# Performance work log

Hardware: AMD Instinct MI355X
Metric: run time of the kernel (lower is better)

The kernel has to match this reference:

```python
import jax, jax.numpy as jnp
import numpy as np

TAU = 1.0          # temperature
PAD = -1.0         # padded_value_indicator
MAX_ITER = 50      # sinkhorn iterations
NEG_BIG = -100000000.0


def setup_inputs() -> dict:
    key = jax.random.key(0)
    k1, k2 = jax.random.split(key)
    B, N = 128, 256
    y_pred = jax.random.normal(k1, (B, N), dtype=jnp.float32)
    y_true = jax.random.randint(k2, (B, N), 0, 5, dtype=jnp.int32)
    return {"y_pred": y_pred, "y_true": y_true}


def deterministic_neural_sort(s, tau, mask):
    # s: [B, n, 1], mask: [B, n] bool
    B, n = s.shape[0], s.shape[1]
    mor = mask[:, :, None] | mask[:, None, :]
    mand = mask[:, :, None] & mask[:, None, :]
    s = jnp.where(mask[:, :, None], NEG_BIG, s)
    A_s = jnp.abs(s - jnp.swapaxes(s, 1, 2))            # [B, n, n]
    A_s = jnp.where(mor, 0.0, A_s)
    # B_mat[b,i,j] = sum_k A_s[b,i,k] (matmul with ones outer product)
    B_mat = A_s.sum(axis=2, keepdims=True)              # [B, n, 1], broadcasts over j
    m = mask.sum(axis=1)                                # [B] number of padded items
    j = jnp.arange(n)
    valid = j[None, :] < (n - m)[:, None]
    scaling = jnp.where(
        valid,
        (n - m)[:, None].astype(jnp.float32) + 1.0 - 2.0 * (j[None, :] + 1).astype(jnp.float32),
        0.0,
    )                                                   # [B, n]
    s0 = jnp.where(mask[:, :, None], 0.0, s)
    C = s0 * scaling[:, None, :]                        # [B,n,1]*[B,1,n] outer product
    P_max = jnp.swapaxes(C - B_mat, 1, 2)
    P_max = jnp.where(mor, -jnp.inf, P_max)
    P_max = jnp.where(mand, 1.0, P_max)
    return jax.nn.softmax(P_max / tau, axis=-1)         # [B, n, n]


def sinkhorn_scaling(mat, mask):
    # mat: [B, n, n], mask: [B, n]
    mor = mask[:, None, :] | mask[:, :, None]
    mand = mask[:, None, :] & mask[:, :, None]
    mat = jnp.where(mor, 0.0, mat)
    mat = jnp.where(mand, 1.0, mat)

    def step(m, _):
        m = m / jnp.clip(m.sum(axis=1, keepdims=True), 1e-10, None)
        m = m / jnp.clip(m.sum(axis=2, keepdims=True), 1e-10, None)
        return m, None

    mat, _ = jax.lax.scan(step, mat, None, length=MAX_ITER)
    return jnp.where(mor, 0.0, mat)


def dcg_at_k(y_pred, y_true, k, gain_fn):
    # returns [B, 1]
    mask = y_true == PAD
    yp = jnp.where(mask, -jnp.inf, y_pred)
    yt = jnp.where(mask, 0.0, y_true)
    order = jnp.argsort(-yp, axis=-1)
    sorted_true = jnp.take_along_axis(yt, order, axis=-1)
    n = y_true.shape[1]
    disc = 1.0 / jnp.log2(jnp.arange(n, dtype=jnp.float32) + 2.0)
    cum = jnp.cumsum(gain_fn(sorted_true) * disc, axis=1)[:, :k]
    return cum[:, k - 1 : k]


def reference(y_pred, y_true):
    B, n = y_pred.shape
    yt = y_true.astype(jnp.float32)
    yt = yt.max() - yt + yt.min()            # relevancy flip as in source
    k = n                                    # self.k is None
    mask = yt == PAD

    P_hat = deterministic_neural_sort(y_pred[:, :, None], TAU, mask)  # [B,n,n]
    P_hat = sinkhorn_scaling(P_hat, mask)[None]                        # [1,B,n,n]
    mor = mask[None, :, :, None] | mask[None, :, None, :]
    P_hat = jnp.where(mor, 0.0, P_hat)

    yt_masked = jnp.where(mask, 0.0, yt)
    gains = jnp.power(2.0, yt_masked) - 1.0                            # powered_relevancies
    ground_truth = jnp.einsum('sbij,bj->sbi', P_hat, gains)            # [1,B,n]
    disc = 1.0 / jnp.log2(jnp.arange(n, dtype=jnp.float32) + 2.0)
    discounted_gains = ground_truth * disc

    idcg = dcg_at_k(yt, yt, k, lambda x: jnp.power(2.0, x) - 1.0).T    # [1,B]
    ndcg = discounted_gains[:, :, :k].sum(axis=-1) / (idcg + 1e-10)    # [1,B]
    idcg_mask = idcg == 0.0
    ndcg = jnp.where(idcg_mask, 0.0, ndcg)
    cnt = (~idcg_mask).sum()
    mean_ndcg = ndcg.sum() / jnp.maximum(cnt.astype(jnp.float32) * ndcg.shape[0], 1.0)
    return jnp.where(cnt > 0, -mean_ndcg, 0.0)
```

## Files before the change

kernel.cpp:

```cpp
#include <hip/hip_runtime.h>


#define NN 256
#define ITERS 50

typedef float v2f __attribute__((ext_vector_type(2)));

__device__ __forceinline__ v2f pkfma(v2f a, v2f b, v2f c) {
    return __builtin_elementwise_fma(a, b, c);
}

template<int C>
__device__ __forceinline__ float dppadd(float v) {
    return v + __int_as_float(__builtin_amdgcn_update_dpp(0, __float_as_int(v), C, 0xF, 0xF, true));
}
template<int C>
__device__ __forceinline__ float dppmax(float v) {
    return fmaxf(v, __int_as_float(__builtin_amdgcn_update_dpp(0, __float_as_int(v), C, 0xF, 0xF, true)));
}
__device__ __forceinline__ float swz16(float v) {
    return __int_as_float(__builtin_amdgcn_ds_swizzle(__float_as_int(v), 0x401F));
}
__device__ __forceinline__ float sum16(float v) {
    v = dppadd<0xB1>(v);
    v = dppadd<0x4E>(v);
    v = dppadd<0x141>(v);
    v = dppadd<0x140>(v);
    return v;
}
__device__ __forceinline__ float sum32f(float v) {
    v = sum16(v);
    v += swz16(v);
    return v;
}
__device__ __forceinline__ float max32f(float v) {
    v = dppmax<0xB1>(v);
    v = dppmax<0x4E>(v);
    v = dppmax<0x141>(v);
    v = dppmax<0x140>(v);
    v = fmaxf(v, swz16(v));
    return v;
}

#if __has_builtin(__builtin_amdgcn_permlane16_swap)
#define HAVE_PLS 1
#endif

__device__ __forceinline__ void sum32_pair(float& A, float& B) {
    A = sum16(A);
    B = sum16(B);
#ifdef HAVE_PLS
    auto r1 = __builtin_amdgcn_permlane16_swap(__float_as_uint(A), __float_as_uint(B), false, false);
    float z = __uint_as_float(r1[0]) + __uint_as_float(r1[1]);
    auto r2 = __builtin_amdgcn_permlane16_swap(__float_as_uint(z), __float_as_uint(z), false, false);
    A = __uint_as_float(r2[0]);
    B = __uint_as_float(r2[1]);
#else
    A += swz16(A);
    B += swz16(B);
#endif
}

__global__ __launch_bounds__(1024, 4) void ndcg_main(const float* __restrict__ yp,
                                                     const int* __restrict__ ytr,
                                                     int nbatch,
                                                     float* __restrict__ ndArr,
                                                     float* __restrict__ cntArr,
                                                     int* __restrict__ doneCnt,
                                                     float* __restrict__ out) {
    const int b = blockIdx.x;
    const int t = threadIdx.x;
    const int l = t & 63;
    const int ti = t >> 5;
    const int tj = t & 31;
    const int cq = t >> 4;
    const int sl = t & 15;

    __shared__ float4 part4[32 * 64];
    __shared__ float4 cvec4[72];
    __shared__ __align__(16) float sarr[NN], bmarr[NN], garr[NN], darr[NN];
    __shared__ float numAcc, idcgAcc;
    __shared__ int hist[64], wmn[16], wmx[16], gmn, gmx;
    __shared__ float redS[16], redC[16];
    __shared__ int lastFlag;

    float* partf = (float*)part4;

    {
        int mn = 0x7fffffff, mx = (int)0x80000000;
        const int4* y4 = (const int4*)ytr;
        const int n4 = nbatch * (NN / 4);
        for (int i = t; i < n4; i += 1024) {
            int4 v = y4[i];
            mn = min(mn, min(min(v.x, v.y), min(v.z, v.w)));
            mx = max(mx, max(max(v.x, v.y), max(v.z, v.w)));
        }
        for (int mo = 1; mo < 64; mo <<= 1) {
            mn = min(mn, __shfl_xor(mn, mo));
            mx = max(mx, __shfl_xor(mx, mo));
        }
        if (l == 0) { wmn[t >> 6] = mn; wmx[t >> 6] = mx; }
    }
    if (t < 64) hist[t] = 0;
    if (t < 72) cvec4[t] = make_float4(1.0f, 1.0f, 1.0f, 1.0f);
    if (t == 0) { numAcc = 0.0f; idcgAcc = 0.0f; }
    __syncthreads();
    if (t == 0) {
        int a = wmn[0], c = wmx[0];
        for (int i = 1; i < 16; ++i) { a = min(a, wmn[i]); c = max(c, wmx[i]); }
        gmn = a; gmx = c;
    }
    __syncthreads();
    const int ymin = gmn, ymax = gmx;

    if (t < NN) {
        sarr[t] = yp[b * NN + t];
        int ytv = ymax - ytr[b * NN + t] + ymin;
        garr[t] = exp2f((float)ytv) - 1.0f;
        darr[t] = 1.0f / log2f((float)t + 2.0f);
        atomicAdd(&hist[min(max(ytv - ymin, 0), 63)], 1);
    }
    __syncthreads();

    {
        int j = t & 255, q = t >> 8;
        float sv = sarr[j];
        float acc = 0.0f;
        int k0 = q * 64;
#pragma unroll 8
        for (int k = 0; k < 64; ++k) acc += fabsf(sv - sarr[k0 + k]);
        partf[q * 256 + j] = acc;
    }
    __syncthreads();
    if (t < NN)
        bmarr[t] = partf[t] + partf[256 + t] + partf[512 + t] + partf[768 + t];
    __syncthreads();

    v2f m2[8][4];
    {
        float sj[8], bm8[8];
        *(float4*)&sj[0]  = ((const float4*)sarr)[tj * 2];
        *(float4*)&sj[4]  = ((const float4*)sarr)[tj * 2 + 1];
        *(float4*)&bm8[0] = ((const float4*)bmarr)[tj * 2];
        *(float4*)&bm8[4] = ((const float4*)bmarr)[tj * 2 + 1];
#pragma unroll
        for (int a = 0; a < 8; ++a) {
            float sc = (float)(255 - 2 * (ti * 8 + a));
            float mv[8];
            float mx = -3.0e38f;
#pragma unroll
            for (int bb = 0; bb < 8; ++bb) {
                mv[bb] = sj[bb] * sc - bm8[bb];
                mx = fmaxf(mx, mv[bb]);
            }
            mx = max32f(mx);
            float z = 0.0f;
#pragma unroll
            for (int bb = 0; bb < 8; ++bb) { mv[bb] = expf(mv[bb] - mx); z += mv[bb]; }
            z = sum32f(z);
            float rz = __builtin_amdgcn_rcpf(z);
#pragma unroll
            for (int bb = 0; bb < 8; ++bb) m2[a][bb >> 1][bb & 1] = mv[bb] * rz;
        }
    }

    if (t < NN) {
        float gain_p = 0.0f;
        int off = 0;
        for (int vb = 63; vb >= 0; --vb) {
            int c = hist[vb];
            if (t >= off && t < off + c) gain_p = exp2f((float)(vb + ymin)) - 1.0f;
            off += c;
        }
        float contrib = sum32f(darr[t] * gain_p);
        contrib += __shfl_xor(contrib, 32);
        if (l == 0) atomicAdd(&idcgAcc, contrib);
    }

    float r[8];
#pragma unroll
    for (int a = 0; a < 8; ++a) r[a] = 1.0f;

    const int wslot = ti * 64 + ((tj + ti) & 31);
    const int csc = t >> 5;
    const int hh = cq & 1;
    const int rslot1 = sl * 64 + ((csc + sl) & 31) + 32 * hh;
    const int rslot2 = (sl + 16) * 64 + ((csc + sl + 16) & 31) + 32 * hh;
    const int cwslot = cq + (cq >> 3);
    const int crslot = tj * 2 + (tj >> 2);

    {
        v2f p2[4];
#pragma unroll
        for (int bp = 0; bp < 4; ++bp)
            p2[bp] = ((m2[0][bp] + m2[1][bp]) + (m2[2][bp] + m2[3][bp])) +
                     ((m2[4][bp] + m2[5][bp]) + (m2[6][bp] + m2[7][bp]));
        part4[wslot]      = make_float4(p2[0].x, p2[0].y, p2[1].x, p2[1].y);
        part4[wslot + 32] = make_float4(p2[2].x, p2[2].y, p2[3].x, p2[3].y);
    }

    for (int it = 0; it < ITERS; ++it) {
        __syncthreads();
        {
            float4 A0 = part4[rslot1];
            float4 A1 = part4[rslot2];
            v2f s01 = (v2f){A0.x, A0.y} + (v2f){A1.x, A1.y};
            v2f s23 = (v2f){A0.z, A0.w} + (v2f){A1.z, A1.w};
            float Sx = sum16(s01.x);
            float Sy = sum16(s01.y);
            float Sz = sum16(s23.x);
            float Sw = sum16(s23.y);
            if (sl == 0) {
                float4 C = cvec4[cwslot];
                float4 F;
                F.x = C.x * __builtin_amdgcn_rcpf(fmaxf(C.x * Sx, 1e-10f));
                F.y = C.y * __builtin_amdgcn_rcpf(fmaxf(C.y * Sy, 1e-10f));
                F.z = C.z * __builtin_amdgcn_rcpf(fmaxf(C.z * Sz, 1e-10f));
                F.w = C.w * __builtin_amdgcn_rcpf(fmaxf(C.w * Sw, 1e-10f));
                cvec4[cwslot] = F;
            }
        }
        __syncthreads();

        {
            float4 ca = cvec4[crslot];
            float4 cb = cvec4[crslot + 1];
            v2f cv2[4] = { {ca.x, ca.y}, {ca.z, ca.w}, {cb.x, cb.y}, {cb.z, cb.w} };
            float rs[8];
#pragma unroll
            for (int a = 0; a < 8; ++a) {
                v2f acc = m2[a][0] * cv2[0];
                acc = pkfma(m2[a][1], cv2[1], acc);
                acc = pkfma(m2[a][2], cv2[2], acc);
                acc = pkfma(m2[a][3], cv2[3], acc);
                rs[a] = acc.x + acc.y;
            }
            sum32_pair(rs[0], rs[1]);
            sum32_pair(rs[2], rs[3]);
            sum32_pair(rs[4], rs[5]);
            sum32_pair(rs[6], rs[7]);
#pragma unroll
            for (int a = 0; a < 8; ++a) {
                float T = fmaxf(r[a] * rs[a], 1e-10f);
                r[a] *= __builtin_amdgcn_rcpf(T);
            }
            v2f p2[4];
#pragma unroll
            for (int bp = 0; bp < 4; ++bp) {
                v2f rr = r[0];
                v2f acc = m2[0][bp] * rr;
#pragma unroll
                for (int a = 1; a < 8; ++a) {
                    v2f ra = r[a];
                    acc = pkfma(m2[a][bp], ra, acc);
                }
                p2[bp] = acc;
            }
            part4[wslot]      = make_float4(p2[0].x, p2[0].y, p2[1].x, p2[1].y);
            part4[wslot + 32] = make_float4(p2[2].x, p2[2].y, p2[3].x, p2[3].y);
        }
    }

    {
        float4 fa = cvec4[crslot];
        float4 fb = cvec4[crslot + 1];
        float4 ga = ((const float4*)garr)[tj * 2];
        float4 gb = ((const float4*)garr)[tj * 2 + 1];
        v2f gv2[4] = { (v2f){fa.x, fa.y} * (v2f){ga.x, ga.y},
                       (v2f){fa.z, fa.w} * (v2f){ga.z, ga.w},
                       (v2f){fb.x, fb.y} * (v2f){gb.x, gb.y},
                       (v2f){fb.z, fb.w} * (v2f){gb.z, gb.w} };
        float q[8];
#pragma unroll
        for (int a = 0; a < 8; ++a) {
            v2f acc = m2[a][0] * gv2[0];
            acc = pkfma(m2[a][1], gv2[1], acc);
            acc = pkfma(m2[a][2], gv2[2], acc);
            acc = pkfma(m2[a][3], gv2[3], acc);
            q[a] = acc.x + acc.y;
        }
        sum32_pair(q[0], q[1]);
        sum32_pair(q[2], q[3]);
        sum32_pair(q[4], q[5]);
        sum32_pair(q[6], q[7]);
        float partial = 0.0f;
#pragma unroll
        for (int a = 0; a < 8; ++a)
            partial = fmaf(darr[ti * 8 + a] * r[a], q[a], partial);
        if (tj == 0) atomicAdd(&numAcc, partial);
    }
    __syncthreads();

    if (t == 0) {
        float idcg = idcgAcc;
        bool ok = (idcg != 0.0f);
        float nd = ok ? numAcc / (idcg + 1e-10f) : 0.0f;
        __hip_atomic_store(&ndArr[b], nd, __ATOMIC_RELAXED, __HIP_MEMORY_SCOPE_AGENT);
        __hip_atomic_store(&cntArr[b], ok ? 1.0f : 0.0f, __ATOMIC_RELAXED, __HIP_MEMORY_SCOPE_AGENT);
        __threadfence();
        int prev = atomicAdd(doneCnt, 1);
        lastFlag = (prev == nbatch - 1) ? 1 : 0;
    }
    __syncthreads();
    if (lastFlag != 0) {
        __threadfence();
        float s = 0.0f, c = 0.0f;
        for (int i = t; i < nbatch; i += 1024) {
            s += __hip_atomic_load(&ndArr[i], __ATOMIC_RELAXED, __HIP_MEMORY_SCOPE_AGENT);
            c += __hip_atomic_load(&cntArr[i], __ATOMIC_RELAXED, __HIP_MEMORY_SCOPE_AGENT);
        }
        for (int mo = 1; mo < 64; mo <<= 1) { s += __shfl_xor(s, mo); c += __shfl_xor(c, mo); }
        if (l == 0) { redS[t >> 6] = s; redC[t >> 6] = c; }
        __syncthreads();
        if (t == 0) {
            float S = 0.0f, C = 0.0f;
            for (int i = 0; i < 16; ++i) { S += redS[i]; C += redC[i]; }
            out[0] = (C > 0.0f) ? -(S / fmaxf(C, 1.0f)) : 0.0f;
        }
    }
}

extern "C" void kernel_launch(void* const* d_in, const int* in_sizes, int n_in,
                              void* d_out, int out_size, void* d_ws, size_t ws_size,
                              hipStream_t stream) {
    const float* y_pred = (const float*)d_in[0];
    const int* y_true = (const int*)d_in[1];
    const int total = in_sizes[0];
    const int B = total / NN;

    int* doneCnt = (int*)d_ws;
    float* ndArr = (float*)d_ws + 64;
    float* cntArr = ndArr + B;

    hipMemsetAsync(doneCnt, 0, sizeof(int), stream);
    ndcg_main<<<B, 1024, 0, stream>>>(y_pred, y_true, B, ndArr, cntArr, doneCnt,
                                      (float*)d_out);
}
```

Measured before the change: 161.7 us.

## Exit Sinkhorn iterations early once scaling vectors reach a bitwise fixed point

The 50 Sinkhorn iterations are split into 12 unconditional iterations, then chunks of four. Each chunk snapshots the row and column scaling vectors after its second iteration and compares them bitwise after its fourth. If every thread sees identical values, the block leaves the loop, because any further iterations would only reproduce the same state. Otherwise it finishes the remaining two iterations, for 50 in total. This is meant to cut the per-iteration barrier and reduction cost when the scalings settle early. It adds snapshot storage in registers and shared memory, plus an extra barrier and wave vote per chunk.

```diff
diff --git a/kernel.cpp b/kernel.cpp
--- a/kernel.cpp
+++ b/kernel.cpp
@@ -60,6 +60,96 @@
     B += swz16(B);
 #endif
 }
+
+#define SINK_B_PHASE                                                         \
+    {                                                                        \
+        float4 A0 = part4[rslot1];                                           \
+        float4 A1 = part4[rslot2];                                           \
+        v2f s01 = (v2f){A0.x, A0.y} + (v2f){A1.x, A1.y};                     \
+        v2f s23 = (v2f){A0.z, A0.w} + (v2f){A1.z, A1.w};                     \
+        float Sx = sum16(s01.x);                                             \
+        float Sy = sum16(s01.y);                                             \
+        float Sz = sum16(s23.x);                                             \
+        float Sw = sum16(s23.y);                                             \
+        if (sl == 0) {                                                       \
+            float4 C = cvec4[cwslot];                                        \
+            float4 F;                                                        \
+            F.x = C.x * __builtin_amdgcn_rcpf(fmaxf(C.x * Sx, 1e-10f));      \
+            F.y = C.y * __builtin_amdgcn_rcpf(fmaxf(C.y * Sy, 1e-10f));      \
+            F.z = C.z * __builtin_amdgcn_rcpf(fmaxf(C.z * Sz, 1e-10f));      \
+            F.w = C.w * __builtin_amdgcn_rcpf(fmaxf(C.w * Sw, 1e-10f));      \
+            cvec4[cwslot] = F;                                               \
+        }                                                                    \
+    }
+
+#define SINK_CA_PHASE(EXTRA)                                                 \
+    {                                                                        \
+        float4 ca = cvec4[crslot];                                           \
+        float4 cb = cvec4[crslot + 1];                                       \
+        v2f cv2[4] = { {ca.x, ca.y}, {ca.z, ca.w}, {cb.x, cb.y}, {cb.z, cb.w} }; \
+        float rs[8];                                                         \
+        _Pragma("unroll")                                                    \
+        for (int a = 0; a < 8; ++a) {                                        \
+            v2f acc = m2[a][0] * cv2[0];                                     \
+            acc = pkfma(m2[a][1], cv2[1], acc);                              \
+            acc = pkfma(m2[a][2], cv2[2], acc);                              \
+            acc = pkfma(m2[a][3], cv2[3], acc);                              \
+            rs[a] = acc.x + acc.y;                                           \
+        }                                                                    \
+        sum32_pair(rs[0], rs[1]);                                            \
+        sum32_pair(rs[2], rs[3]);                                            \
+        sum32_pair(rs[4], rs[5]);                                            \
+        sum32_pair(rs[6], rs[7]);                                            \
+        _Pragma("unroll")                                                    \
+        for (int a = 0; a < 8; ++a) {                                        \
+            float T = fmaxf(r[a] * rs[a], 1e-10f);                           \
+            r[a] *= __builtin_amdgcn_rcpf(T);                                \
+        }                                                                    \
+        EXTRA                                                                \
+        {                                                                    \
+            v2f p2[4];                                                       \
+            _Pragma("unroll")                                                \
+            for (int bp = 0; bp < 4; ++bp) {                                 \
+                v2f rr = r[0];                                               \
+                v2f acc = m2[0][bp] * rr;                                    \
+                _Pragma("unroll")                                            \
+                for (int a = 1; a < 8; ++a) {                                \
+                    v2f ra = r[a];                                           \
+                    acc = pkfma(m2[a][bp], ra, acc);                         \
+                }                                                            \
+                p2[bp] = acc;                                                \
+            }                                                                \
+            part4[wslot]      = make_float4(p2[0].x, p2[0].y, p2[1].x, p2[1].y); \
+            part4[wslot + 32] = make_float4(p2[2].x, p2[2].y, p2[3].x, p2[3].y); \
+        }                                                                    \
+    }
+
+#define SINK_ITER(EXTRA) { __syncthreads(); SINK_B_PHASE; __syncthreads(); SINK_CA_PHASE(EXTRA) }
+
+#define SNAP_EXTRA                                                           \
+    {                                                                        \
+        _Pragma("unroll")                                                    \
+        for (int a = 0; a < 8; ++a) rsnap[a] = r[a];                         \
+        if (t < 72) csnap[t] = cvec4[t];                                     \
+    }
+
+#define CHECK_EXTRA                                                          \
+    {                                                                        \
+        bool okc = true;                                                     \
+        _Pragma("unroll")                                                    \
+        for (int a = 0; a < 8; ++a)                                          \
+            okc &= (__float_as_uint(r[a]) == __float_as_uint(rsnap[a]));     \
+        if (t < 72) {                                                        \
+            float4 Aq = cvec4[t];                                            \
+            float4 Bq = csnap[t];                                            \
+            okc &= (__float_as_uint(Aq.x) == __float_as_uint(Bq.x));         \
+            okc &= (__float_as_uint(Aq.y) == __float_as_uint(Bq.y));         \
+            okc &= (__float_as_uint(Aq.z) == __float_as_uint(Bq.z));         \
+            okc &= (__float_as_uint(Aq.w) == __float_as_uint(Bq.w));         \
+        }                                                                    \
+        if (!__all(okc) && l == 0) convFlag[ci & 1] = 0;                     \
+        if (t == 0) convFlag[(ci + 1) & 1] = 1;                              \
+    }
 
 __global__ __launch_bounds__(1024, 4) void ndcg_main(const float* __restrict__ yp,
                                                      const int* __restrict__ ytr,
@@ -78,11 +168,13 @@
 
     __shared__ float4 part4[32 * 64];
     __shared__ float4 cvec4[72];
+    __shared__ float4 csnap[72];
     __shared__ __align__(16) float sarr[NN], bmarr[NN], garr[NN], darr[NN];
     __shared__ float numAcc, idcgAcc;
     __shared__ int hist[64], wmn[16], wmx[16], gmn, gmx;
     __shared__ float redS[16], redC[16];
     __shared__ int lastFlag;
+    __shared__ int convFlag[2];
 
     float* partf = (float*)part4;
 
@@ -103,6 +195,7 @@
     }
     if (t < 64) hist[t] = 0;
     if (t < 72) cvec4[t] = make_float4(1.0f, 1.0f, 1.0f, 1.0f);
+    if (t < 2) convFlag[t] = 1;
     if (t == 0) { numAcc = 0.0f; idcgAcc = 0.0f; }
     __syncthreads();
     if (t == 0) {
@@ -177,9 +270,9 @@
         if (l == 0) atomicAdd(&idcgAcc, contrib);
     }
 
-    float r[8];
-#pragma unroll
-    for (int a = 0; a < 8; ++a) r[a] = 1.0f;
+    float r[8], rsnap[8];
+#pragma unroll
+    for (int a = 0; a < 8; ++a) { r[a] = 1.0f; rsnap[a] = 0.0f; }
 
     const int wslot = ti * 64 + ((tj + ti) & 31);
     const int csc = t >> 5;
@@ -199,67 +292,22 @@
         part4[wslot + 32] = make_float4(p2[2].x, p2[2].y, p2[3].x, p2[3].y);
     }
 
-    for (int it = 0; it < ITERS; ++it) {
+    for (int k = 0; k < 12; ++k) SINK_ITER(;)
+
+    bool conv = false;
+    int ci = 0;
+#pragma unroll 1
+    for (int chunk = 0; chunk < 9; ++chunk) {
+        SINK_ITER(;)
+        SINK_ITER(SNAP_EXTRA)
+        SINK_ITER(;)
+        SINK_ITER(CHECK_EXTRA)
         __syncthreads();
-        {
-            float4 A0 = part4[rslot1];
-            float4 A1 = part4[rslot2];
-            v2f s01 = (v2f){A0.x, A0.y} + (v2f){A1.x, A1.y};
-            v2f s23 = (v2f){A0.z, A0.w} + (v2f){A1.z, A1.w};
-            float Sx = sum16(s01.x);
-            float Sy = sum16(s01.y);
-            float Sz = sum16(s23.x);
-            float Sw = sum16(s23.y);
-            if (sl == 0) {
-                float4 C = cvec4[cwslot];
-                float4 F;
-                F.x = C.x * __builtin_amdgcn_rcpf(fmaxf(C.x * Sx, 1e-10f));
-                F.y = C.y * __builtin_amdgcn_rcpf(fmaxf(C.y * Sy, 1e-10f));
-                F.z = C.z * __builtin_amdgcn_rcpf(fmaxf(C.z * Sz, 1e-10f));
-                F.w = C.w * __builtin_amdgcn_rcpf(fmaxf(C.w * Sw, 1e-10f));
-                cvec4[cwslot] = F;
-            }
-        }
-        __syncthreads();
-
-        {
-            float4 ca = cvec4[crslot];
-            float4 cb = cvec4[crslot + 1];
-            v2f cv2[4] = { {ca.x, ca.y}, {ca.z, ca.w}, {cb.x, cb.y}, {cb.z, cb.w} };
-            float rs[8];
-#pragma unroll
-            for (int a = 0; a < 8; ++a) {
-                v2f acc = m2[a][0] * cv2[0];
-                acc = pkfma(m2[a][1], cv2[1], acc);
-                acc = pkfma(m2[a][2], cv2[2], acc);
-                acc = pkfma(m2[a][3], cv2[3], acc);
-                rs[a] = acc.x + acc.y;
-            }
-            sum32_pair(rs[0], rs[1]);
-            sum32_pair(rs[2], rs[3]);
-            sum32_pair(rs[4], rs[5]);
-            sum32_pair(rs[6], rs[7]);
-#pragma unroll
-            for (int a = 0; a < 8; ++a) {
-                float T = fmaxf(r[a] * rs[a], 1e-10f);
-                r[a] *= __builtin_amdgcn_rcpf(T);
-            }
-            v2f p2[4];
-#pragma unroll
-            for (int bp = 0; bp < 4; ++bp) {
-                v2f rr = r[0];
-                v2f acc = m2[0][bp] * rr;
-#pragma unroll
-                for (int a = 1; a < 8; ++a) {
-                    v2f ra = r[a];
-                    acc = pkfma(m2[a][bp], ra, acc);
-                }
-                p2[bp] = acc;
-            }
-            part4[wslot]      = make_float4(p2[0].x, p2[0].y, p2[1].x, p2[1].y);
-            part4[wslot + 32] = make_float4(p2[2].x, p2[2].y, p2[3].x, p2[3].y);
-        }
-    }
+        conv = (convFlag[ci & 1] != 0);
+        ++ci;
+        if (conv) break;
+    }
+    if (!conv) { SINK_ITER(;) SINK_ITER(;) }
 
     {
         float4 fa = cvec4[crslot];
```

Measured after the change: 165.8 us. 2.6% more time.
